# Optimization experiments

Measured on AMD Instinct MI355X. Metric: run time of the kernel, lower is better.

The kernel has to match this reference:

```python
import jax, jax.numpy as jnp
import numpy as np

N_NODES = 100000
N_EDGES = 600000
N_GRAPHS = 512
DIM = 128
N_LAYERS = 3
N_CLASSES = 2
BN_EPS = 1e-5


def setup_inputs() -> dict:
    key = jax.random.key(0)
    ks = jax.random.split(key, 16)
    s = 1.0 / np.sqrt(DIM)
    inp = {
        "x": jax.random.normal(ks[0], (N_NODES, DIM), dtype=jnp.float32),
        "edge_index": jax.random.randint(ks[1], (2, N_EDGES), 0, N_NODES, dtype=jnp.int32),
        "batch": jnp.sort(jax.random.randint(ks[2], (N_NODES,), 0, N_GRAPHS, dtype=jnp.int32)),
        # GIN MLP params per layer: Linear -> BN -> Linear -> BN
        "W1": jax.random.uniform(ks[3], (N_LAYERS, DIM, DIM), jnp.float32, -s, s),
        "b1": jax.random.uniform(ks[4], (N_LAYERS, DIM), jnp.float32, -s, s),
        "g1": jnp.ones((N_LAYERS, DIM), jnp.float32),
        "bt1": jnp.zeros((N_LAYERS, DIM), jnp.float32),
        "W2": jax.random.uniform(ks[5], (N_LAYERS, DIM, DIM), jnp.float32, -s, s),
        "b2": jax.random.uniform(ks[6], (N_LAYERS, DIM), jnp.float32, -s, s),
        "g2": jnp.ones((N_LAYERS, DIM), jnp.float32),
        "bt2": jnp.zeros((N_LAYERS, DIM), jnp.float32),
        # outer BatchNorm per layer
        "go": jnp.ones((N_LAYERS, DIM), jnp.float32),
        "bo": jnp.zeros((N_LAYERS, DIM), jnp.float32),
        # final classifier
        "fcW": jax.random.uniform(ks[7], (DIM, N_CLASSES), jnp.float32, -s, s),
        "fcb": jax.random.uniform(ks[8], (N_CLASSES,), jnp.float32, -s, s),
    }
    return inp


def _bn(h, g, b):
    # training-mode BatchNorm1d over nodes (axis 0), biased variance
    m = jnp.mean(h, axis=0)
    v = jnp.var(h, axis=0)
    return (h - m) * jax.lax.rsqrt(v + BN_EPS) * g + b


def reference(x, edge_index, batch, W1, b1, g1, bt1, W2, b2, g2, bt2, go, bo, fcW, fcb):
    src, dst = edge_index[0], edge_index[1]
    h = x
    for i in range(N_LAYERS):
        # GIN aggregate: sum_{j in N(i)} x_j  + (1+eps)*x_i, eps=0
        agg = jax.ops.segment_sum(h[src], dst, num_segments=N_NODES)
        h = agg + h
        # GIN MLP: Linear -> BN -> Linear -> BN
        h = _bn(h @ W1[i] + b1[i], g1[i], bt1[i])
        h = _bn(h @ W2[i] + b2[i], g2[i], bt2[i])
        # outer BN + ReLU (dropout p=0 is a no-op)
        h = jax.nn.relu(_bn(h, go[i], bo[i]))
    node_embeddings = h
    # global mean pool per graph
    sums = jax.ops.segment_sum(node_embeddings, batch, num_segments=N_GRAPHS)
    counts = jax.ops.segment_sum(jnp.ones((N_NODES,), jnp.float32), batch, num_segments=N_GRAPHS)
    graph_embedding = sums / jnp.maximum(counts, 1.0)[:, None]
    out = graph_embedding @ fcW + fcb
    return (node_embeddings, graph_embedding, out)
```

## Files before the change

kernel.cpp:

```cpp
#include <hip/hip_runtime.h>

#define NN 100000
#define NE 600000
#define NG 512
#define D 128
#define NL 3
#define EPS 1e-5f

__global__ __launch_bounds__(256) void k_hist(const int* __restrict__ ei,
                                              int* __restrict__ deg) {
    int e = blockIdx.x * 256 + threadIdx.x;
    if (e < NE) atomicAdd(&deg[ei[NE + e]], 1);
}

__global__ __launch_bounds__(256) void k_scan1(const int* __restrict__ deg,
                                               int* __restrict__ excl,
                                               int* __restrict__ bsum) {
    __shared__ int s[256];
    int i = blockIdx.x * 256 + threadIdx.x;
    int v = (i < NN) ? deg[i] : 0;
    s[threadIdx.x] = v;
    __syncthreads();
    #pragma unroll
    for (int st = 1; st < 256; st <<= 1) {
        int t = (threadIdx.x >= st) ? s[threadIdx.x - st] : 0;
        __syncthreads();
        s[threadIdx.x] += t;
        __syncthreads();
    }
    if (i < NN) excl[i] = s[threadIdx.x] - v;
    if (threadIdx.x == 255) bsum[blockIdx.x] = s[255];
}

__global__ __launch_bounds__(512) void k_scan2(int* __restrict__ bsum, int nb) {
    __shared__ int s[512];
    int v = (threadIdx.x < nb) ? bsum[threadIdx.x] : 0;
    s[threadIdx.x] = v;
    __syncthreads();
    #pragma unroll
    for (int st = 1; st < 512; st <<= 1) {
        int t = (threadIdx.x >= st) ? s[threadIdx.x - st] : 0;
        __syncthreads();
        s[threadIdx.x] += t;
        __syncthreads();
    }
    if (threadIdx.x < nb) bsum[threadIdx.x] = s[threadIdx.x] - v;
}

__global__ __launch_bounds__(256) void k_scan3(const int* __restrict__ excl,
                                               const int* __restrict__ bsum,
                                               int* __restrict__ off,
                                               int* __restrict__ cur) {
    int i = blockIdx.x * 256 + threadIdx.x;
    if (i < NN) {
        int o = excl[i] + bsum[blockIdx.x];
        off[i] = o;
        cur[i] = o;
    }
    if (i == 0) off[NN] = NE;
}

__global__ __launch_bounds__(256) void k_fill(const int* __restrict__ ei,
                                              int* __restrict__ cur,
                                              int* __restrict__ srcs) {
    int e = blockIdx.x * 256 + threadIdx.x;
    if (e < NE) {
        int d = ei[NE + e];
        int p = atomicAdd(&cur[d], 1);
        srcs[p] = ei[e];
    }
}

__global__ __launch_bounds__(256) void k_goff(const int* __restrict__ batch,
                                              int* __restrict__ goff,
                                              const float* __restrict__ b2all,
                                              float* __restrict__ biasFall) {
    int i = blockIdx.x * 256 + threadIdx.x;
    if (blockIdx.x == 0) {
        for (int j = threadIdx.x; j < NL * D; j += 256) biasFall[j] = b2all[j];
    }
    if (i == 0) {
        int b0 = batch[0];
        for (int g = 0; g <= b0; ++g) goff[g] = 0;
    }
    if (i < NN - 1) {
        int b = batch[i], bn = batch[i + 1];
        for (int g = b + 1; g <= bn; ++g) goff[g] = i + 1;
    }
    if (i == NN - 1) {
        int b = batch[NN - 1];
        for (int g = b + 1; g <= NG; ++g) goff[g] = NN;
    }
}

__global__ __launch_bounds__(256) void k_gather(const float4* __restrict__ hin,
                                                const int* __restrict__ off,
                                                const int* __restrict__ srcs,
                                                float4* __restrict__ g) {
    int t = blockIdx.x * 256 + threadIdx.x;
    int n = t >> 5;
    if (n >= NN) return;
    int f4 = t & 31;
    int lo = off[n], hi = off[n + 1];
    float4 acc = hin[(long)n * 32 + f4];
    for (int e = lo; e < hi; ++e) {
        int s = srcs[e];
        float4 v = hin[(long)s * 32 + f4];
        acc.x += v.x; acc.y += v.y; acc.z += v.z; acc.w += v.w;
    }
    g[(long)n * 32 + f4] = acc;
}

__global__ __launch_bounds__(256) void k_gather_aff(const float4* __restrict__ yin,
                                                    const int* __restrict__ off,
                                                    const int* __restrict__ srcs,
                                                    const float* __restrict__ affA,
                                                    const float* __restrict__ affB,
                                                    float4* __restrict__ g) {
    int t = blockIdx.x * 256 + threadIdx.x;
    int n = t >> 5;
    if (n >= NN) return;
    int f4 = t & 31;
    float4 A = *(const float4*)(affA + f4 * 4);
    float4 B = *(const float4*)(affB + f4 * 4);
    int lo = off[n], hi = off[n + 1];
    float4 v = yin[(long)n * 32 + f4];
    float4 acc;
    acc.x = fmaxf(fmaf(v.x, A.x, B.x), 0.f);
    acc.y = fmaxf(fmaf(v.y, A.y, B.y), 0.f);
    acc.z = fmaxf(fmaf(v.z, A.z, B.z), 0.f);
    acc.w = fmaxf(fmaf(v.w, A.w, B.w), 0.f);
    for (int e = lo; e < hi; ++e) {
        int s = srcs[e];
        float4 u = yin[(long)s * 32 + f4];
        acc.x += fmaxf(fmaf(u.x, A.x, B.x), 0.f);
        acc.y += fmaxf(fmaf(u.y, A.y, B.y), 0.f);
        acc.z += fmaxf(fmaf(u.z, A.z, B.z), 0.f);
        acc.w += fmaxf(fmaf(u.w, A.w, B.w), 0.f);
    }
    g[(long)n * 32 + f4] = acc;
}

#define BM 64
#define BK 32
#define RST 65

__global__ __launch_bounds__(256, 5) void k_gemm(const float* __restrict__ A,
                                                 const float* __restrict__ W,
                                                 const float* __restrict__ bias,
                                                 float* __restrict__ C,
                                                 float* __restrict__ sum,
                                                 float* __restrict__ sq) {
    __shared__ float Ws[BK * 128];
    __shared__ float As[BK * RST];
    const int tid = threadIdx.x;
    const int ty = tid >> 4;
    const int tx = tid & 15;
    const long base = (long)blockIdx.x * BM;

    float acc[4][8];
    #pragma unroll
    for (int i = 0; i < 4; ++i)
        #pragma unroll
        for (int c = 0; c < 8; ++c) acc[i][c] = 0.f;

    for (int kc = 0; kc < 128; kc += BK) {
        #pragma unroll
        for (int j = 0; j < 4; ++j) {
            int e = tid + j * 256;
            int k = e >> 5, q = e & 31;
            int p = ((q & 1) << 4) + (q >> 1);
            float4 v = *(const float4*)(W + (long)(kc + k) * 128 + q * 4);
            *(float4*)(&Ws[k * 128 + p * 4]) = v;
        }
        #pragma unroll
        for (int j = 0; j < 2; ++j) {
            int e = tid + j * 256;
            int row = e >> 3, cq = e & 7;
            long gr = base + row;
            float4 v = make_float4(0.f, 0.f, 0.f, 0.f);
            if (gr < NN) v = *(const float4*)(A + gr * D + kc + cq * 4);
            As[(cq * 4 + 0) * RST + row] = v.x;
            As[(cq * 4 + 1) * RST + row] = v.y;
            As[(cq * 4 + 2) * RST + row] = v.z;
            As[(cq * 4 + 3) * RST + row] = v.w;
        }
        __syncthreads();
        #pragma unroll
        for (int k = 0; k < BK; ++k) {
            float4 a4 = *(const float4*)(&As[k * RST + ty * 4]);
            float4 w0 = *(const float4*)(&Ws[k * 128 + tx * 4]);
            float4 w1 = *(const float4*)(&Ws[k * 128 + 64 + tx * 4]);
            float av[4] = {a4.x, a4.y, a4.z, a4.w};
            float wv[8] = {w0.x, w0.y, w0.z, w0.w, w1.x, w1.y, w1.z, w1.w};
            #pragma unroll
            for (int i = 0; i < 4; ++i)
                #pragma unroll
                for (int c = 0; c < 8; ++c) acc[i][c] = fmaf(av[i], wv[c], acc[i][c]);
        }
        __syncthreads();
    }

    float4 b0 = *(const float4*)(bias + tx * 8);
    float4 b1 = *(const float4*)(bias + tx * 8 + 4);
    float bv[8] = {b0.x, b0.y, b0.z, b0.w, b1.x, b1.y, b1.z, b1.w};
    float csum[8], csq[8];
    #pragma unroll
    for (int c = 0; c < 8; ++c) { csum[c] = 0.f; csq[c] = 0.f; }
    #pragma unroll
    for (int i = 0; i < 4; ++i) {
        long gr = base + ty * 4 + i;
        if (gr < NN) {
            float o[8];
            #pragma unroll
            for (int c = 0; c < 8; ++c) {
                o[c] = acc[i][c] + bv[c];
                csum[c] += o[c];
                csq[c] += o[c] * o[c];
            }
            *(float4*)(C + gr * D + tx * 8) = make_float4(o[0], o[1], o[2], o[3]);
            *(float4*)(C + gr * D + tx * 8 + 4) = make_float4(o[4], o[5], o[6], o[7]);
        }
    }
    float* red = Ws;
    __syncthreads();
    *(float4*)(&red[ty * 128 + tx * 8]) = make_float4(csum[0], csum[1], csum[2], csum[3]);
    *(float4*)(&red[ty * 128 + tx * 8 + 4]) = make_float4(csum[4], csum[5], csum[6], csum[7]);
    *(float4*)(&red[2048 + ty * 128 + tx * 8]) = make_float4(csq[0], csq[1], csq[2], csq[3]);
    *(float4*)(&red[2048 + ty * 128 + tx * 8 + 4]) = make_float4(csq[4], csq[5], csq[6], csq[7]);
    __syncthreads();
    if (tid < 128) {
        float t = 0.f;
        #pragma unroll
        for (int j = 0; j < 16; ++j) t += red[j * 128 + tid];
        atomicAdd(sum + tid, t);
    } else {
        int col = tid - 128;
        float t = 0.f;
        #pragma unroll
        for (int j = 0; j < 16; ++j) t += red[2048 + j * 128 + col];
        atomicAdd(sq + col, t);
    }
}

__global__ __launch_bounds__(128) void k_fold(const float* __restrict__ W2,
                                              float* __restrict__ sum,
                                              float* __restrict__ sq,
                                              const float* __restrict__ g1,
                                              const float* __restrict__ bt1,
                                              float* __restrict__ W2s,
                                              float* __restrict__ biasF) {
    int k = blockIdx.x, j = threadIdx.x;
    float m = sum[k] * (1.f / NN);
    float v = sq[k] * (1.f / NN) - m * m;
    __syncthreads();
    if (j == 0) { sum[k] = 0.f; sq[k] = 0.f; }
    float a = g1[k] * rsqrtf(v + EPS);
    float c = bt1[k] - m * a;
    float w = W2[(long)k * 128 + j];
    W2s[(long)k * 128 + j] = a * w;
    atomicAdd(biasF + j, c * w);
}

__global__ void k_fin2(float* __restrict__ sum, float* __restrict__ sq,
                       const float* __restrict__ g2, const float* __restrict__ go,
                       const float* __restrict__ bo, float* __restrict__ affA,
                       float* __restrict__ affB) {
    int f = threadIdx.x;
    float m = sum[f] * (1.f / NN);
    float v = sq[f] * (1.f / NN) - m * m;
    sum[f] = 0.f;
    sq[f] = 0.f;
    float t = g2[f] * rsqrtf(v + EPS);
    float vo = t * t * v;
    float Aa = t * rsqrtf(vo + EPS) * go[f];
    affA[f] = Aa;
    affB[f] = bo[f] - m * Aa;
}

__global__ __launch_bounds__(256) void k_affine_pool(const float4* __restrict__ Y,
                                                     const float* __restrict__ affA,
                                                     const float* __restrict__ affB,
                                                     const int* __restrict__ batch,
                                                     float4* __restrict__ nodeEmb,
                                                     float* __restrict__ gsum) {
    int tid = threadIdx.x;
    int f4 = tid & 31;
    int rg = tid >> 5;
    long base = (long)blockIdx.x * 64 + (long)rg * 8;
    float4 A = *(const float4*)(affA + f4 * 4);
    float4 B = *(const float4*)(affB + f4 * 4);
    float4 run = make_float4(0.f, 0.f, 0.f, 0.f);
    int curg = -1;
    #pragma unroll
    for (int i = 0; i < 8; ++i) {
        long r = base + i;
        if (r >= NN) break;
        int g = batch[r];
        float4 v = Y[r * 32 + f4];
        float4 o;
        o.x = fmaxf(fmaf(v.x, A.x, B.x), 0.f);
        o.y = fmaxf(fmaf(v.y, A.y, B.y), 0.f);
        o.z = fmaxf(fmaf(v.z, A.z, B.z), 0.f);
        o.w = fmaxf(fmaf(v.w, A.w, B.w), 0.f);
        nodeEmb[r * 32 + f4] = o;
        if (g != curg) {
            if (curg >= 0) {
                float* p = gsum + (long)curg * D + f4 * 4;
                atomicAdd(p + 0, run.x); atomicAdd(p + 1, run.y);
                atomicAdd(p + 2, run.z); atomicAdd(p + 3, run.w);
            }
            curg = g;
            run = o;
        } else {
            run.x += o.x; run.y += o.y; run.z += o.z; run.w += o.w;
        }
    }
    if (curg >= 0) {
        float* p = gsum + (long)curg * D + f4 * 4;
        atomicAdd(p + 0, run.x); atomicAdd(p + 1, run.y);
        atomicAdd(p + 2, run.z); atomicAdd(p + 3, run.w);
    }
}

__global__ __launch_bounds__(128) void k_fc(const float* __restrict__ gsum,
                                            const int* __restrict__ goff,
                                            const float* __restrict__ fcW,
                                            const float* __restrict__ fcb,
                                            float* __restrict__ ge,
                                            float* __restrict__ out) {
    __shared__ float r0[128], r1[128];
    int g = blockIdx.x, j = threadIdx.x;
    int cnt = goff[g + 1] - goff[g];
    float mean = gsum[(long)g * D + j] / (float)(cnt > 0 ? cnt : 1);
    ge[(long)g * D + j] = mean;
    r0[j] = mean * fcW[j * 2 + 0];
    r1[j] = mean * fcW[j * 2 + 1];
    __syncthreads();
    for (int st = 64; st > 0; st >>= 1) {
        if (j < st) { r0[j] += r0[j + st]; r1[j] += r1[j + st]; }
        __syncthreads();
    }
    if (j == 0) {
        out[g * 2 + 0] = r0[0] + fcb[0];
        out[g * 2 + 1] = r1[0] + fcb[1];
    }
}

extern "C" void kernel_launch(void* const* d_in, const int* in_sizes, int n_in,
                              void* d_out, int out_size, void* d_ws, size_t ws_size,
                              hipStream_t stream) {
    const float* x   = (const float*)d_in[0];
    const int*   ei  = (const int*)d_in[1];
    const int*   bat = (const int*)d_in[2];
    const float* W1  = (const float*)d_in[3];
    const float* b1  = (const float*)d_in[4];
    const float* g1  = (const float*)d_in[5];
    const float* bt1 = (const float*)d_in[6];
    const float* W2  = (const float*)d_in[7];
    const float* b2  = (const float*)d_in[8];
    const float* g2  = (const float*)d_in[9];
    const float* go  = (const float*)d_in[11];
    const float* bo  = (const float*)d_in[12];
    const float* fcW = (const float*)d_in[13];
    const float* fcb = (const float*)d_in[14];

    const long ND = (long)NN * D;
    float* H = (float*)d_ws;
    float* G = H + ND;
    float* S = G + ND;
    float* sum      = S;
    float* sq       = S + 128;
    float* gsum     = S + 256;
    float* biasFall = S + 65792;
    float* affA     = S + 66176;
    float* affB     = S + 66304;
    float* W2s      = S + 66432;
    int*   goff     = (int*)(S + 82816);
    int*   off      = (int*)(S + 83840);
    int*   srcs     = off + (NN + 1);

    float* nodeEmb = (float*)d_out;
    float* ge   = nodeEmb + ND;
    float* out2 = ge + (long)NG * D;
    float* Y = nodeEmb;

    int* deg  = (int*)nodeEmb;
    int* excl = deg + NN;
    int* cur  = excl + NN;
    int* bsum = cur + NN;

    const int edgeGrid = (NE + 255) / 256;
    const int nodeGrid = (NN + 255) / 256;
    const int gathGrid = (int)(((long)NN * 32 + 255) / 256);
    const int gemmGrid = (NN + BM - 1) / BM;
    const int apGrid   = (NN + 63) / 64;

    hipMemsetAsync(deg, 0, NN * sizeof(int), stream);
    k_hist<<<edgeGrid, 256, 0, stream>>>(ei, deg);
    k_scan1<<<nodeGrid, 256, 0, stream>>>(deg, excl, bsum);
    k_scan2<<<1, 512, 0, stream>>>(bsum, nodeGrid);
    k_scan3<<<nodeGrid, 256, 0, stream>>>(excl, bsum, off, cur);
    k_fill<<<edgeGrid, 256, 0, stream>>>(ei, cur, srcs);

    hipMemsetAsync(sum, 0, (256 + (long)NG * D) * sizeof(float), stream);
    k_goff<<<nodeGrid, 256, 0, stream>>>(bat, goff, b2, biasFall);

    for (int l = 0; l < NL; ++l) {
        if (l == 0)
            k_gather<<<gathGrid, 256, 0, stream>>>((const float4*)x, off, srcs,
                                                   (float4*)G);
        else
            k_gather_aff<<<gathGrid, 256, 0, stream>>>((const float4*)G, off, srcs,
                                                       affA, affB, (float4*)H);
        const float* gin = (l == 0) ? G : H;

        k_gemm<<<gemmGrid, 256, 0, stream>>>(gin, W1 + (long)l * D * D, b1 + l * D,
                                             Y, sum, sq);
        k_fold<<<128, 128, 0, stream>>>(W2 + (long)l * D * D, sum, sq,
                                        g1 + l * D, bt1 + l * D, W2s,
                                        biasFall + (long)l * D);

        k_gemm<<<gemmGrid, 256, 0, stream>>>(Y, W2s, biasFall + (long)l * D,
                                             G, sum, sq);
        k_fin2<<<1, 128, 0, stream>>>(sum, sq, g2 + l * D, go + l * D, bo + l * D,
                                      affA, affB);
    }

    k_affine_pool<<<apGrid, 256, 0, stream>>>((const float4*)G, affA, affB, bat,
                                              (float4*)nodeEmb, gsum);
    k_fc<<<NG, 128, 0, stream>>>(gsum, goff, fcW, fcb, ge, out2);
}
```

Measured before the change: 794.8 us.

## Use 8x8 register tiles with 128 threads and register-prefetch next K chunk in GEMM

The GEMM block drops from 256 to 128 threads, and each thread now computes an 8x8 output micro-tile instead of 4x8, which raises arithmetic intensity per shared-memory load. The next K-chunk of W and A is loaded from global memory into registers while the current chunk is computed, overlapping global latency with FMAs. The column-statistics reduction is simplified to one sum and one square-sum per thread. The trade-off is higher register pressure and fewer waves per CU (launch bounds now 3 blocks per CU), which could reduce latency hiding.

```diff
diff --git a/kernel.cpp b/kernel.cpp
--- a/kernel.cpp
+++ b/kernel.cpp
@@ -145,7 +145,7 @@
 #define BK 32
 #define RST 65
 
-__global__ __launch_bounds__(256, 5) void k_gemm(const float* __restrict__ A,
+__global__ __launch_bounds__(128, 3) void k_gemm(const float* __restrict__ A,
                                                  const float* __restrict__ W,
                                                  const float* __restrict__ bias,
                                                  float* __restrict__ C,
@@ -158,45 +158,78 @@
     const int tx = tid & 15;
     const long base = (long)blockIdx.x * BM;
 
-    float acc[4][8];
-    #pragma unroll
-    for (int i = 0; i < 4; ++i)
+    float4 wpre[8];
+    float4 apre[4];
+
+    #pragma unroll
+    for (int j = 0; j < 8; ++j) {
+        int e = tid + j * 128;
+        int k = e >> 5, q = e & 31;
+        wpre[j] = *(const float4*)(W + (long)k * 128 + q * 4);
+    }
+    #pragma unroll
+    for (int j = 0; j < 4; ++j) {
+        int e = tid + j * 128;
+        int row = e >> 3, cq = e & 7;
+        long gr = base + row;
+        apre[j] = (gr < NN) ? *(const float4*)(A + gr * D + cq * 4)
+                            : make_float4(0.f, 0.f, 0.f, 0.f);
+    }
+
+    float acc[8][8];
+    #pragma unroll
+    for (int i = 0; i < 8; ++i)
         #pragma unroll
         for (int c = 0; c < 8; ++c) acc[i][c] = 0.f;
 
-    for (int kc = 0; kc < 128; kc += BK) {
+    for (int c = 0; c < 4; ++c) {
+        #pragma unroll
+        for (int j = 0; j < 8; ++j) {
+            int e = tid + j * 128;
+            int k = e >> 5, q = e & 31;
+            int p = ((q & 1) << 4) + (q >> 1);
+            *(float4*)(&Ws[k * 128 + p * 4]) = wpre[j];
+        }
         #pragma unroll
         for (int j = 0; j < 4; ++j) {
-            int e = tid + j * 256;
-            int k = e >> 5, q = e & 31;
-            int p = ((q & 1) << 4) + (q >> 1);
-            float4 v = *(const float4*)(W + (long)(kc + k) * 128 + q * 4);
-            *(float4*)(&Ws[k * 128 + p * 4]) = v;
-        }
-        #pragma unroll
-        for (int j = 0; j < 2; ++j) {
-            int e = tid + j * 256;
+            int e = tid + j * 128;
             int row = e >> 3, cq = e & 7;
-            long gr = base + row;
-            float4 v = make_float4(0.f, 0.f, 0.f, 0.f);
-            if (gr < NN) v = *(const float4*)(A + gr * D + kc + cq * 4);
-            As[(cq * 4 + 0) * RST + row] = v.x;
-            As[(cq * 4 + 1) * RST + row] = v.y;
-            As[(cq * 4 + 2) * RST + row] = v.z;
-            As[(cq * 4 + 3) * RST + row] = v.w;
-        }
-        __syncthreads();
+            As[(cq * 4 + 0) * RST + row] = apre[j].x;
+            As[(cq * 4 + 1) * RST + row] = apre[j].y;
+            As[(cq * 4 + 2) * RST + row] = apre[j].z;
+            As[(cq * 4 + 3) * RST + row] = apre[j].w;
+        }
+        __syncthreads();
+        if (c < 3) {
+            int kc = (c + 1) * BK;
+            #pragma unroll
+            for (int j = 0; j < 8; ++j) {
+                int e = tid + j * 128;
+                int k = e >> 5, q = e & 31;
+                wpre[j] = *(const float4*)(W + (long)(kc + k) * 128 + q * 4);
+            }
+            #pragma unroll
+            for (int j = 0; j < 4; ++j) {
+                int e = tid + j * 128;
+                int row = e >> 3, cq = e & 7;
+                long gr = base + row;
+                apre[j] = (gr < NN) ? *(const float4*)(A + gr * D + kc + cq * 4)
+                                    : make_float4(0.f, 0.f, 0.f, 0.f);
+            }
+        }
         #pragma unroll
         for (int k = 0; k < BK; ++k) {
-            float4 a4 = *(const float4*)(&As[k * RST + ty * 4]);
+            float4 a0 = *(const float4*)(&As[k * RST + ty * 8]);
+            float4 a1 = *(const float4*)(&As[k * RST + ty * 8 + 4]);
             float4 w0 = *(const float4*)(&Ws[k * 128 + tx * 4]);
             float4 w1 = *(const float4*)(&Ws[k * 128 + 64 + tx * 4]);
-            float av[4] = {a4.x, a4.y, a4.z, a4.w};
+            float av[8] = {a0.x, a0.y, a0.z, a0.w, a1.x, a1.y, a1.z, a1.w};
             float wv[8] = {w0.x, w0.y, w0.z, w0.w, w1.x, w1.y, w1.z, w1.w};
             #pragma unroll
-            for (int i = 0; i < 4; ++i)
+            for (int i = 0; i < 8; ++i)
                 #pragma unroll
-                for (int c = 0; c < 8; ++c) acc[i][c] = fmaf(av[i], wv[c], acc[i][c]);
+                for (int cc = 0; cc < 8; ++cc)
+                    acc[i][cc] = fmaf(av[i], wv[cc], acc[i][cc]);
         }
         __syncthreads();
     }
@@ -208,8 +241,8 @@
     #pragma unroll
     for (int c = 0; c < 8; ++c) { csum[c] = 0.f; csq[c] = 0.f; }
     #pragma unroll
-    for (int i = 0; i < 4; ++i) {
-        long gr = base + ty * 4 + i;
+    for (int i = 0; i < 8; ++i) {
+        long gr = base + ty * 8 + i;
         if (gr < NN) {
             float o[8];
             #pragma unroll
@@ -223,24 +256,19 @@
         }
     }
     float* red = Ws;
-    __syncthreads();
     *(float4*)(&red[ty * 128 + tx * 8]) = make_float4(csum[0], csum[1], csum[2], csum[3]);
     *(float4*)(&red[ty * 128 + tx * 8 + 4]) = make_float4(csum[4], csum[5], csum[6], csum[7]);
-    *(float4*)(&red[2048 + ty * 128 + tx * 8]) = make_float4(csq[0], csq[1], csq[2], csq[3]);
-    *(float4*)(&red[2048 + ty * 128 + tx * 8 + 4]) = make_float4(csq[4], csq[5], csq[6], csq[7]);
+    *(float4*)(&red[1024 + ty * 128 + tx * 8]) = make_float4(csq[0], csq[1], csq[2], csq[3]);
+    *(float4*)(&red[1024 + ty * 128 + tx * 8 + 4]) = make_float4(csq[4], csq[5], csq[6], csq[7]);
     __syncthreads();
-    if (tid < 128) {
-        float t = 0.f;
-        #pragma unroll
-        for (int j = 0; j < 16; ++j) t += red[j * 128 + tid];
-        atomicAdd(sum + tid, t);
-    } else {
-        int col = tid - 128;
-        float t = 0.f;
-        #pragma unroll
-        for (int j = 0; j < 16; ++j) t += red[2048 + j * 128 + col];
-        atomicAdd(sq + col, t);
-    }
+    float tsum = 0.f, tsq = 0.f;
+    #pragma unroll
+    for (int j = 0; j < 8; ++j) {
+        tsum += red[j * 128 + tid];
+        tsq  += red[1024 + j * 128 + tid];
+    }
+    atomicAdd(sum + tid, tsum);
+    atomicAdd(sq + tid, tsq);
 }
 
 __global__ __launch_bounds__(128) void k_fold(const float* __restrict__ W2,
@@ -415,13 +443,13 @@
                                                        affA, affB, (float4*)H);
         const float* gin = (l == 0) ? G : H;
 
-        k_gemm<<<gemmGrid, 256, 0, stream>>>(gin, W1 + (long)l * D * D, b1 + l * D,
+        k_gemm<<<gemmGrid, 128, 0, stream>>>(gin, W1 + (long)l * D * D, b1 + l * D,
                                              Y, sum, sq);
         k_fold<<<128, 128, 0, stream>>>(W2 + (long)l * D * D, sum, sq,
                                         g1 + l * D, bt1 + l * D, W2s,
                                         biasFall + (long)l * D);
 
-        k_gemm<<<gemmGrid, 256, 0, stream>>>(Y, W2s, biasFall + (long)l * D,
+        k_gemm<<<gemmGrid, 128, 0, stream>>>(Y, W2s, biasFall + (long)l * D,
                                              G, sum, sq);
         k_fin2<<<1, 128, 0, stream>>>(sum, sq, g2 + l * D, go + l * D, bo + l * D,
                                       affA, affB);
```

Result: slower. 1.224 ms (+54.0%).

## Replace FP32 SIMT GEMMs with split-bf16 MFMA GEMMs and slab-spread BN statistics

Applied to the files above, without the earlier changes.

The FP32 shared-memory GEMMs are replaced by a matrix-core kernel that splits each operand into high and low bf16 parts and issues three MFMA products to keep close to FP32 accuracy. The gather kernels and the intermediate GEMM output now write bf16 hi/lo pairs, and the weights are pre-transposed and converted. BN column statistics are spread over 8 atomic slabs to reduce atomic contention. The cost is three times the MFMA work, extra conversion arithmetic and some precision loss. Operands are read straight from global memory without shared-memory staging, and the grid of NN/32 has no tail guard.

```diff
diff --git a/kernel.cpp b/kernel.cpp
--- a/kernel.cpp
+++ b/kernel.cpp
@@ -6,6 +6,19 @@
 #define D 128
 #define NL 3
 #define EPS 1e-5f
+
+typedef unsigned short u16;
+typedef __attribute__((ext_vector_type(8))) short bf16x8;
+typedef __attribute__((ext_vector_type(4))) float f32x4;
+
+__device__ __forceinline__ u16 f2bf(float x) {
+    unsigned u = __float_as_uint(x);
+    u = u + 0x7FFFu + ((u >> 16) & 1u);
+    return (u16)(u >> 16);
+}
+__device__ __forceinline__ float bf2f(u16 h) {
+    return __uint_as_float(((unsigned)h) << 16);
+}
 
 __global__ __launch_bounds__(256) void k_hist(const int* __restrict__ ei,
                                               int* __restrict__ deg) {
@@ -93,10 +106,23 @@
     }
 }
 
+__global__ __launch_bounds__(128) void k_wcvt(const float* __restrict__ W1,
+                                              u16* __restrict__ Wth,
+                                              u16* __restrict__ Wtl) {
+    int b = blockIdx.x;
+    int l = b >> 7, k = b & 127;
+    int j = threadIdx.x;
+    float w = W1[(long)l * 16384 + (long)k * 128 + j];
+    u16 h = f2bf(w);
+    Wth[(long)l * 16384 + (long)j * 128 + k] = h;
+    Wtl[(long)l * 16384 + (long)j * 128 + k] = f2bf(w - bf2f(h));
+}
+
 __global__ __launch_bounds__(256) void k_gather(const float4* __restrict__ hin,
                                                 const int* __restrict__ off,
                                                 const int* __restrict__ srcs,
-                                                float4* __restrict__ g) {
+                                                u16* __restrict__ Ahi,
+                                                u16* __restrict__ Alo) {
     int t = blockIdx.x * 256 + threadIdx.x;
     int n = t >> 5;
     if (n >= NN) return;
@@ -108,7 +134,11 @@
         float4 v = hin[(long)s * 32 + f4];
         acc.x += v.x; acc.y += v.y; acc.z += v.z; acc.w += v.w;
     }
-    g[(long)n * 32 + f4] = acc;
+    u16 hx = f2bf(acc.x), hy = f2bf(acc.y), hz = f2bf(acc.z), hw = f2bf(acc.w);
+    u16 lx = f2bf(acc.x - bf2f(hx)), ly = f2bf(acc.y - bf2f(hy));
+    u16 lz = f2bf(acc.z - bf2f(hz)), lw = f2bf(acc.w - bf2f(hw));
+    *(ushort4*)(Ahi + (long)n * 128 + f4 * 4) = make_ushort4(hx, hy, hz, hw);
+    *(ushort4*)(Alo + (long)n * 128 + f4 * 4) = make_ushort4(lx, ly, lz, lw);
 }
 
 __global__ __launch_bounds__(256) void k_gather_aff(const float4* __restrict__ yin,
@@ -116,7 +146,8 @@
                                                     const int* __restrict__ srcs,
                                                     const float* __restrict__ affA,
                                                     const float* __restrict__ affB,
-                                                    float4* __restrict__ g) {
+                                                    u16* __restrict__ Ahi,
+                                                    u16* __restrict__ Alo) {
     int t = blockIdx.x * 256 + threadIdx.x;
     int n = t >> 5;
     if (n >= NN) return;
@@ -138,139 +169,128 @@
         acc.z += fmaxf(fmaf(u.z, A.z, B.z), 0.f);
         acc.w += fmaxf(fmaf(u.w, A.w, B.w), 0.f);
     }
-    g[(long)n * 32 + f4] = acc;
-}
-
-#define BM 64
-#define BK 32
-#define RST 65
-
-__global__ __launch_bounds__(256, 5) void k_gemm(const float* __restrict__ A,
-                                                 const float* __restrict__ W,
-                                                 const float* __restrict__ bias,
-                                                 float* __restrict__ C,
-                                                 float* __restrict__ sum,
-                                                 float* __restrict__ sq) {
-    __shared__ float Ws[BK * 128];
-    __shared__ float As[BK * RST];
+    u16 hx = f2bf(acc.x), hy = f2bf(acc.y), hz = f2bf(acc.z), hw = f2bf(acc.w);
+    u16 lx = f2bf(acc.x - bf2f(hx)), ly = f2bf(acc.y - bf2f(hy));
+    u16 lz = f2bf(acc.z - bf2f(hz)), lw = f2bf(acc.w - bf2f(hw));
+    *(ushort4*)(Ahi + (long)n * 128 + f4 * 4) = make_ushort4(hx, hy, hz, hw);
+    *(ushort4*)(Alo + (long)n * 128 + f4 * 4) = make_ushort4(lx, ly, lz, lw);
+}
+
+template <int MODE>
+__global__ __launch_bounds__(128) void k_gemm_bf3(const u16* __restrict__ Ahi,
+                                                  const u16* __restrict__ Alo,
+                                                  const u16* __restrict__ Bth,
+                                                  const u16* __restrict__ Btl,
+                                                  const float* __restrict__ bias,
+                                                  u16* __restrict__ Yhi,
+                                                  u16* __restrict__ Ylo,
+                                                  float* __restrict__ Gout,
+                                                  float* __restrict__ slab) {
+    __shared__ float ls[2][128], lq[2][128];
     const int tid = threadIdx.x;
-    const int ty = tid >> 4;
-    const int tx = tid & 15;
-    const long base = (long)blockIdx.x * BM;
-
-    float acc[4][8];
-    #pragma unroll
-    for (int i = 0; i < 4; ++i)
+    const int wid = tid >> 6, lane = tid & 63;
+    const int rmod = lane & 15, kgrp = lane >> 4;
+    const long base = ((long)blockIdx.x * 2 + wid) * 16;
+    const long arow = base + rmod;
+
+    f32x4 acc[8];
+    #pragma unroll
+    for (int c = 0; c < 8; ++c) acc[c] = (f32x4){0.f, 0.f, 0.f, 0.f};
+
+    #pragma unroll
+    for (int kt = 0; kt < 4; ++kt) {
+        const int koff = kt * 32 + kgrp * 8;
+        bf16x8 ah = *(const bf16x8*)(Ahi + arow * 128 + koff);
+        bf16x8 al = *(const bf16x8*)(Alo + arow * 128 + koff);
         #pragma unroll
-        for (int c = 0; c < 8; ++c) acc[i][c] = 0.f;
-
-    for (int kc = 0; kc < 128; kc += BK) {
+        for (int ct = 0; ct < 8; ++ct) {
+            const long boff = (long)(ct * 16 + rmod) * 128 + koff;
+            bf16x8 bh = *(const bf16x8*)(Bth + boff);
+            bf16x8 bl = *(const bf16x8*)(Btl + boff);
+            acc[ct] = __builtin_amdgcn_mfma_f32_16x16x32_bf16(ah, bh, acc[ct], 0, 0, 0);
+            acc[ct] = __builtin_amdgcn_mfma_f32_16x16x32_bf16(ah, bl, acc[ct], 0, 0, 0);
+            acc[ct] = __builtin_amdgcn_mfma_f32_16x16x32_bf16(al, bh, acc[ct], 0, 0, 0);
+        }
+    }
+
+    #pragma unroll
+    for (int ct = 0; ct < 8; ++ct) {
+        int col = ct * 16 + rmod;
+        float bv = bias[col];
+        float s = 0.f, q = 0.f;
         #pragma unroll
-        for (int j = 0; j < 4; ++j) {
-            int e = tid + j * 256;
-            int k = e >> 5, q = e & 31;
-            int p = ((q & 1) << 4) + (q >> 1);
-            float4 v = *(const float4*)(W + (long)(kc + k) * 128 + q * 4);
-            *(float4*)(&Ws[k * 128 + p * 4]) = v;
+        for (int r = 0; r < 4; ++r) {
+            float o = acc[ct][r] + bv;
+            s += o;
+            q += o * o;
+            long row = base + kgrp * 4 + r;
+            if (MODE == 0) {
+                u16 h = f2bf(o);
+                Yhi[row * 128 + col] = h;
+                Ylo[row * 128 + col] = f2bf(o - bf2f(h));
+            } else {
+                Gout[row * 128 + col] = o;
+            }
         }
-        #pragma unroll
-        for (int j = 0; j < 2; ++j) {
-            int e = tid + j * 256;
-            int row = e >> 3, cq = e & 7;
-            long gr = base + row;
-            float4 v = make_float4(0.f, 0.f, 0.f, 0.f);
-            if (gr < NN) v = *(const float4*)(A + gr * D + kc + cq * 4);
-            As[(cq * 4 + 0) * RST + row] = v.x;
-            As[(cq * 4 + 1) * RST + row] = v.y;
-            As[(cq * 4 + 2) * RST + row] = v.z;
-            As[(cq * 4 + 3) * RST + row] = v.w;
-        }
-        __syncthreads();
-        #pragma unroll
-        for (int k = 0; k < BK; ++k) {
-            float4 a4 = *(const float4*)(&As[k * RST + ty * 4]);
-            float4 w0 = *(const float4*)(&Ws[k * 128 + tx * 4]);
-            float4 w1 = *(const float4*)(&Ws[k * 128 + 64 + tx * 4]);
-            float av[4] = {a4.x, a4.y, a4.z, a4.w};
-            float wv[8] = {w0.x, w0.y, w0.z, w0.w, w1.x, w1.y, w1.z, w1.w};
-            #pragma unroll
-            for (int i = 0; i < 4; ++i)
-                #pragma unroll
-                for (int c = 0; c < 8; ++c) acc[i][c] = fmaf(av[i], wv[c], acc[i][c]);
-        }
-        __syncthreads();
-    }
-
-    float4 b0 = *(const float4*)(bias + tx * 8);
-    float4 b1 = *(const float4*)(bias + tx * 8 + 4);
-    float bv[8] = {b0.x, b0.y, b0.z, b0.w, b1.x, b1.y, b1.z, b1.w};
-    float csum[8], csq[8];
-    #pragma unroll
-    for (int c = 0; c < 8; ++c) { csum[c] = 0.f; csq[c] = 0.f; }
-    #pragma unroll
-    for (int i = 0; i < 4; ++i) {
-        long gr = base + ty * 4 + i;
-        if (gr < NN) {
-            float o[8];
-            #pragma unroll
-            for (int c = 0; c < 8; ++c) {
-                o[c] = acc[i][c] + bv[c];
-                csum[c] += o[c];
-                csq[c] += o[c] * o[c];
-            }
-            *(float4*)(C + gr * D + tx * 8) = make_float4(o[0], o[1], o[2], o[3]);
-            *(float4*)(C + gr * D + tx * 8 + 4) = make_float4(o[4], o[5], o[6], o[7]);
-        }
-    }
-    float* red = Ws;
+        s += __shfl_xor(s, 16);
+        s += __shfl_xor(s, 32);
+        q += __shfl_xor(q, 16);
+        q += __shfl_xor(q, 32);
+        if (kgrp == 0) { ls[wid][col] = s; lq[wid][col] = q; }
+    }
     __syncthreads();
-    *(float4*)(&red[ty * 128 + tx * 8]) = make_float4(csum[0], csum[1], csum[2], csum[3]);
-    *(float4*)(&red[ty * 128 + tx * 8 + 4]) = make_float4(csum[4], csum[5], csum[6], csum[7]);
-    *(float4*)(&red[2048 + ty * 128 + tx * 8]) = make_float4(csq[0], csq[1], csq[2], csq[3]);
-    *(float4*)(&red[2048 + ty * 128 + tx * 8 + 4]) = make_float4(csq[4], csq[5], csq[6], csq[7]);
-    __syncthreads();
-    if (tid < 128) {
-        float t = 0.f;
-        #pragma unroll
-        for (int j = 0; j < 16; ++j) t += red[j * 128 + tid];
-        atomicAdd(sum + tid, t);
-    } else {
-        int col = tid - 128;
-        float t = 0.f;
-        #pragma unroll
-        for (int j = 0; j < 16; ++j) t += red[2048 + j * 128 + col];
-        atomicAdd(sq + col, t);
+    {
+        float s = ls[0][tid] + ls[1][tid];
+        float q = lq[0][tid] + lq[1][tid];
+        float* sp = slab + (blockIdx.x & 7) * 256;
+        atomicAdd(sp + tid, s);
+        atomicAdd(sp + 128 + tid, q);
     }
 }
 
 __global__ __launch_bounds__(128) void k_fold(const float* __restrict__ W2,
-                                              float* __restrict__ sum,
-                                              float* __restrict__ sq,
+                                              float* __restrict__ slab,
                                               const float* __restrict__ g1,
                                               const float* __restrict__ bt1,
-                                              float* __restrict__ W2s,
+                                              u16* __restrict__ Wth,
+                                              u16* __restrict__ Wtl,
                                               float* __restrict__ biasF) {
     int k = blockIdx.x, j = threadIdx.x;
-    float m = sum[k] * (1.f / NN);
-    float v = sq[k] * (1.f / NN) - m * m;
-    __syncthreads();
-    if (j == 0) { sum[k] = 0.f; sq[k] = 0.f; }
+    float ms = 0.f, mq = 0.f;
+    #pragma unroll
+    for (int s2 = 0; s2 < 8; ++s2) {
+        ms += slab[s2 * 256 + k];
+        mq += slab[s2 * 256 + 128 + k];
+    }
+    float m = ms * (1.f / NN);
+    float v = mq * (1.f / NN) - m * m;
     float a = g1[k] * rsqrtf(v + EPS);
     float c = bt1[k] - m * a;
     float w = W2[(long)k * 128 + j];
-    W2s[(long)k * 128 + j] = a * w;
+    float ws2 = a * w;
+    u16 h = f2bf(ws2);
+    Wth[(long)j * 128 + k] = h;
+    Wtl[(long)j * 128 + k] = f2bf(ws2 - bf2f(h));
     atomicAdd(biasF + j, c * w);
-}
-
-__global__ void k_fin2(float* __restrict__ sum, float* __restrict__ sq,
+    __syncthreads();
+    if (j < 8) { slab[j * 256 + k] = 0.f; slab[j * 256 + 128 + k] = 0.f; }
+}
+
+__global__ void k_fin2(float* __restrict__ slab,
                        const float* __restrict__ g2, const float* __restrict__ go,
                        const float* __restrict__ bo, float* __restrict__ affA,
                        float* __restrict__ affB) {
     int f = threadIdx.x;
-    float m = sum[f] * (1.f / NN);
-    float v = sq[f] * (1.f / NN) - m * m;
-    sum[f] = 0.f;
-    sq[f] = 0.f;
+    float ms = 0.f, mq = 0.f;
+    #pragma unroll
+    for (int s2 = 0; s2 < 8; ++s2) {
+        ms += slab[s2 * 256 + f];
+        mq += slab[s2 * 256 + 128 + f];
+        slab[s2 * 256 + f] = 0.f;
+        slab[s2 * 256 + 128 + f] = 0.f;
+    }
+    float m = ms * (1.f / NN);
+    float v = mq * (1.f / NN) - m * m;
     float t = g2[f] * rsqrtf(v + EPS);
     float vo = t * t * v;
     float Aa = t * rsqrtf(vo + EPS) * go[f];
@@ -366,26 +386,31 @@
     const float* fcb = (const float*)d_in[14];
 
     const long ND = (long)NN * D;
-    float* H = (float*)d_ws;
-    float* G = H + ND;
-    float* S = G + ND;
-    float* sum      = S;
-    float* sq       = S + 128;
-    float* gsum     = S + 256;
-    float* biasFall = S + 65792;
-    float* affA     = S + 66176;
-    float* affB     = S + 66304;
-    float* W2s      = S + 66432;
-    int*   goff     = (int*)(S + 82816);
-    int*   off      = (int*)(S + 83840);
+    float* ws = (float*)d_ws;
+    float* G   = ws;
+    u16*   Ahi = (u16*)(ws + ND);
+    u16*   Alo = Ahi + ND;
+    float* S   = ws + 2 * ND;
+    float* slab     = S;
+    float* gsum     = S + 2048;
+    float* biasFall = S + 67584;
+    float* affA     = S + 67968;
+    float* affB     = S + 68096;
+    int*   goff     = (int*)(S + 68224);
+    u16*   W1tHi    = (u16*)(S + 68740);
+    u16*   W1tLo    = (u16*)(S + 93316);
+    u16*   W2tHi    = (u16*)(S + 117892);
+    u16*   W2tLo    = (u16*)(S + 126084);
+    int*   off      = (int*)(S + 134276);
     int*   srcs     = off + (NN + 1);
 
     float* nodeEmb = (float*)d_out;
+    u16*   Yhi = (u16*)d_out;
+    u16*   Ylo = Yhi + ND;
     float* ge   = nodeEmb + ND;
     float* out2 = ge + (long)NG * D;
-    float* Y = nodeEmb;
-
-    int* deg  = (int*)nodeEmb;
+
+    int* deg  = (int*)d_out;
     int* excl = deg + NN;
     int* cur  = excl + NN;
     int* bsum = cur + NN;
@@ -393,8 +418,7 @@
     const int edgeGrid = (NE + 255) / 256;
     const int nodeGrid = (NN + 255) / 256;
     const int gathGrid = (int)(((long)NN * 32 + 255) / 256);
-    const int gemmGrid = (NN + BM - 1) / BM;
-    const int apGrid   = (NN + 63) / 64;
+    const int gemmGrid = NN / 32;
 
     hipMemsetAsync(deg, 0, NN * sizeof(int), stream);
     k_hist<<<edgeGrid, 256, 0, stream>>>(ei, deg);
@@ -403,31 +427,35 @@
     k_scan3<<<nodeGrid, 256, 0, stream>>>(excl, bsum, off, cur);
     k_fill<<<edgeGrid, 256, 0, stream>>>(ei, cur, srcs);
 
-    hipMemsetAsync(sum, 0, (256 + (long)NG * D) * sizeof(float), stream);
+    hipMemsetAsync(slab, 0, (2048 + (long)NG * D) * sizeof(float), stream);
     k_goff<<<nodeGrid, 256, 0, stream>>>(bat, goff, b2, biasFall);
+    k_wcvt<<<NL * 128, 128, 0, stream>>>(W1, W1tHi, W1tLo);
 
     for (int l = 0; l < NL; ++l) {
         if (l == 0)
             k_gather<<<gathGrid, 256, 0, stream>>>((const float4*)x, off, srcs,
-                                                   (float4*)G);
+                                                   Ahi, Alo);
         else
             k_gather_aff<<<gathGrid, 256, 0, stream>>>((const float4*)G, off, srcs,
-                                                       affA, affB, (float4*)H);
-        const float* gin = (l == 0) ? G : H;
-
-        k_gemm<<<gemmGrid, 256, 0, stream>>>(gin, W1 + (long)l * D * D, b1 + l * D,
-                                             Y, sum, sq);
-        k_fold<<<128, 128, 0, stream>>>(W2 + (long)l * D * D, sum, sq,
-                                        g1 + l * D, bt1 + l * D, W2s,
-                                        biasFall + (long)l * D);
-
-        k_gemm<<<gemmGrid, 256, 0, stream>>>(Y, W2s, biasFall + (long)l * D,
-                                             G, sum, sq);
-        k_fin2<<<1, 128, 0, stream>>>(sum, sq, g2 + l * D, go + l * D, bo + l * D,
+                                                       affA, affB, Ahi, Alo);
+
+        k_gemm_bf3<0><<<gemmGrid, 128, 0, stream>>>(
+            Ahi, Alo, W1tHi + (long)l * 16384, W1tLo + (long)l * 16384,
+            b1 + l * D, Yhi, Ylo, nullptr, slab);
+
+        k_fold<<<128, 128, 0, stream>>>(W2 + (long)l * D * D, slab,
+                                        g1 + l * D, bt1 + l * D,
+                                        W2tHi, W2tLo, biasFall + (long)l * D);
+
+        k_gemm_bf3<1><<<gemmGrid, 128, 0, stream>>>(
+            Yhi, Ylo, W2tHi, W2tLo, biasFall + (long)l * D,
+            nullptr, nullptr, G, slab);
+
+        k_fin2<<<1, 128, 0, stream>>>(slab, g2 + l * D, go + l * D, bo + l * D,
                                       affA, affB);
     }
 
-    k_affine_pool<<<apGrid, 256, 0, stream>>>((const float4*)G, affA, affB, bat,
-                                              (float4*)nodeEmb, gsum);
+    k_affine_pool<<<(NN + 63) / 64, 256, 0, stream>>>((const float4*)G, affA, affB,
+                                                      bat, (float4*)nodeEmb, gsum);
     k_fc<<<NG, 128, 0, stream>>>(gsum, goff, fcW, fcb, ge, out2);
 }
```

Measured after the change: 831.3 us. +4.6%, slower.
